# Performance work log

Hardware: AMD Instinct MI355X
Metric: run time of the kernel (lower is better)

The kernel has to match this reference:

```python
import jax, jax.numpy as jnp
import numpy as np

N = 50000
E = 800000
IN_C = 128
HID = 32
HEADS = 4
G = 512      # number of graphs in batch
OUT_C = 100
NEG_SLOPE = 0.2
EPS = 1e-16


def _gat_params(key, f_in, heads, c):
    k1, k2, k3, k4 = jax.random.split(key, 4)
    s = 1.0 / np.sqrt(f_in)
    return {
        'W': jax.random.uniform(k1, (heads * c, f_in), jnp.float32, -s, s),
        'att_src': jax.random.normal(k2, (heads, c), jnp.float32) * 0.1,
        'att_dst': jax.random.normal(k3, (heads, c), jnp.float32) * 0.1,
        'b': jnp.zeros((heads * c,), jnp.float32),
    }


def setup_inputs() -> dict:
    key = jax.random.key(0)
    ks = jax.random.split(key, 8)
    x = jax.random.normal(ks[0], (N, IN_C), jnp.float32)
    edge_index = jax.random.randint(ks[1], (2, E), 0, N, jnp.int64)
    batch = jnp.sort(jax.random.randint(ks[2], (N,), 0, G, jnp.int64))
    p1 = _gat_params(ks[3], IN_C, HEADS, HID)
    p2 = _gat_params(ks[4], HEADS * HID, HEADS, HID)
    p3 = _gat_params(ks[5], HEADS * HID, HEADS, HID)
    s = 1.0 / np.sqrt(HEADS * HID)
    fc_W = jax.random.uniform(ks[6], (OUT_C, HEADS * HID), jnp.float32, -s, s)
    fc_b = jnp.zeros((OUT_C,), jnp.float32)
    return {
        'x': x, 'edge_index': edge_index, 'batch': batch,
        'W1': p1['W'], 'as1': p1['att_src'], 'ad1': p1['att_dst'], 'b1': p1['b'],
        'W2': p2['W'], 'as2': p2['att_src'], 'ad2': p2['att_dst'], 'b2': p2['b'],
        'W3': p3['W'], 'as3': p3['att_src'], 'ad3': p3['att_dst'], 'b3': p3['b'],
        'fc_W': fc_W, 'fc_b': fc_b,
    }


def gat_conv(x, src, dst, W, att_src, att_dst, b):
    # x: [N, F_in] -> h: [N, H, C]
    h = (x @ W.T).reshape(N, HEADS, HID)
    a_src = jnp.einsum('nhc,hc->nh', h, att_src)   # [N, H]
    a_dst = jnp.einsum('nhc,hc->nh', h, att_dst)
    alpha = a_src[src] + a_dst[dst]                 # [E', H]
    alpha = jax.nn.leaky_relu(alpha, NEG_SLOPE)
    # segment softmax over incoming edges of each dst node
    m = jax.ops.segment_max(alpha, dst, num_segments=N)
    alpha = jnp.exp(alpha - m[dst])
    denom = jax.ops.segment_sum(alpha, dst, num_segments=N)
    alpha = alpha / (denom[dst] + EPS)
    msg = alpha[:, :, None] * h[src]                # [E', H, C]
    out = jax.ops.segment_sum(msg, dst, num_segments=N)
    return out.reshape(N, HEADS * HID) + b


def reference(x, edge_index, batch,
              W1, as1, ad1, b1, W2, as2, ad2, b2, W3, as3, ad3, b3,
              fc_W, fc_b):
    # add self loops (PyG GATConv default)
    loops = jnp.arange(N, dtype=edge_index.dtype)
    src = jnp.concatenate([edge_index[0], loops])
    dst = jnp.concatenate([edge_index[1], loops])
    h = jax.nn.elu(gat_conv(x, src, dst, W1, as1, ad1, b1))
    h = jax.nn.elu(gat_conv(h, src, dst, W2, as2, ad2, b2))
    h = jax.nn.elu(gat_conv(h, src, dst, W3, as3, ad3, b3))
    # global mean pool over graphs
    sums = jax.ops.segment_sum(h, batch, num_segments=G)        # [G, H*C]
    cnts = jax.ops.segment_sum(jnp.ones((N,), h.dtype), batch, num_segments=G)
    pooled = sums / jnp.maximum(cnts, 1.0)[:, None]
    # dropout p=0.5 is identity in eval mode
    return pooled @ fc_W.T + fc_b
```

## Files before the change

### kernel.cpp

```cpp
#include <hip/hip_runtime.h>
#include <math.h>

#define NN 50000
#define EE 800000
#define GG 512
#define OUTC 100
#define NEG 0.2f
#define STRIDE 64
#define NPART 8
#define PRNG (NN / NPART)
#define PCHUNK 4096

typedef __attribute__((ext_vector_type(8))) short bf16x8;
typedef __attribute__((ext_vector_type(8))) short s16x8;
typedef __attribute__((ext_vector_type(8))) unsigned short us8;
typedef __attribute__((ext_vector_type(4))) float f32x4;

__device__ inline ushort f2bf(float v) {
  unsigned u = __float_as_uint(v);
  unsigned r = (u + 0x7fff + ((u >> 16) & 1)) >> 16;
  return (ushort)r;
}

__global__ __launch_bounds__(256) void k_scatter(const int* __restrict__ ei,
    int* __restrict__ cursor, ushort* __restrict__ srcs) {
  int part = blockIdx.x & (NPART - 1);
  int chunk = blockIdx.x >> 3;
  int lo = part * PRNG, hi = lo + PRNG;
  int base = chunk * PCHUNK;
  for (int i = threadIdx.x; i < PCHUNK; i += 256) {
    int e = base + i;
    if (e >= EE) break;
    int d = ei[EE + e];
    if (d < lo || d >= hi) continue;
    int s = ei[e];
    int pos = atomicAdd(&cursor[d], 1);
    if (pos < STRIDE) srcs[(d << 6) + pos] = (ushort)s;
  }
}

__global__ __launch_bounds__(256) void k_prep(
    const float* __restrict__ W0, const float* __restrict__ W1, const float* __restrict__ W2,
    const float* __restrict__ as0, const float* __restrict__ as1, const float* __restrict__ as2,
    const float* __restrict__ ad0, const float* __restrict__ ad1, const float* __restrict__ ad2,
    ushort* __restrict__ hi, ushort* __restrict__ lo) {
  int layer = blockIdx.y;
  const float* W  = (layer == 0) ? W0 : (layer == 1) ? W1 : W2;
  const float* av = (layer == 0) ? as0 : (layer == 1) ? as1 : as2;
  const float* dv = (layer == 0) ? ad0 : (layer == 1) ? ad1 : ad2;
  ushort* hiL = hi + (size_t)layer * 144 * 128;
  ushort* loL = lo + (size_t)layer * 144 * 128;
  int idx = blockIdx.x * 256 + threadIdx.x;
  if (blockIdx.x < 64) {
    float v = W[idx];
    ushort hb = f2bf(v);
    float hf = __uint_as_float(((unsigned)hb) << 16);
    hiL[idx] = hb;
    loL[idx] = f2bf(v - hf);
  } else {
    int j2 = idx - 64 * 256;
    int j = j2 >> 7, k = j2 & 127;
    int head = j & 3;
    const float* vec = (j < 4) ? &av[head * 32] : &dv[head * 32];
    float dot = 0.f;
#pragma unroll
    for (int c = 0; c < 32; c++) dot += W[(head * 32 + c) * 128 + k] * vec[c];
    ushort hb = f2bf(dot);
    float hf = __uint_as_float(((unsigned)hb) << 16);
    hiL[(128 + j) * 128 + k] = hb;
    loL[(128 + j) * 128 + k] = f2bf(dot - hf);
    hiL[(136 + j) * 128 + k] = 0;
    loL[(136 + j) * 128 + k] = 0;
  }
}

__global__ __launch_bounds__(256) void k_gemm_mfma(const float* __restrict__ feat,
    const ushort* __restrict__ Whi, const ushort* __restrict__ Wlo,
    short* __restrict__ hq, float* __restrict__ scalef,
    float* __restrict__ asrcf, float* __restrict__ adstf) {
  __shared__ ushort Ahi[128 * 128];
  __shared__ ushort Alo[128 * 128];
  int n0 = blockIdx.x * 128;
  int t = threadIdx.x;
  {
    int row = t >> 1, half = t & 1;
    int n = n0 + row;
    int sw = row & 15;
    if (n < NN) {
      const float4* src = (const float4*)&feat[(size_t)n * 128 + half * 64];
#pragma unroll
      for (int i = 0; i < 8; i++) {
        float4 a = src[2 * i], b = src[2 * i + 1];
        float vv[8] = {a.x, a.y, a.z, a.w, b.x, b.y, b.z, b.w};
        us8 hh, ll;
#pragma unroll
        for (int j = 0; j < 8; j++) {
          ushort hb = f2bf(vv[j]);
          float hf = __uint_as_float(((unsigned)hb) << 16);
          hh[j] = hb;
          ll[j] = f2bf(vv[j] - hf);
        }
        int pc = (half * 8 + i) ^ sw;
        *(us8*)&Ahi[row * 128 + pc * 8] = hh;
        *(us8*)&Alo[row * 128 + pc * 8] = ll;
      }
    } else {
      us8 z = (us8)0;
#pragma unroll
      for (int i = 0; i < 8; i++) {
        int pc = (half * 8 + i) ^ sw;
        *(us8*)&Ahi[row * 128 + pc * 8] = z;
        *(us8*)&Alo[row * 128 + pc * 8] = z;
      }
    }
  }
  __syncthreads();

  int wave = t >> 6, lane = t & 63;
  int quad = lane >> 4, r16 = lane & 15;
  f32x4 acc[2][8];
#pragma unroll
  for (int mt = 0; mt < 2; mt++)
#pragma unroll
    for (int nt = 0; nt < 8; nt++) acc[mt][nt] = (f32x4)0.f;

  for (int ks = 0; ks < 4; ks++) {
    bf16x8 bh[8], bl[8];
#pragma unroll
    for (int nt = 0; nt < 8; nt++) {
      size_t wo = (size_t)(nt * 16 + r16) * 128 + ks * 32 + quad * 8;
      bh[nt] = *(const bf16x8*)&Whi[wo];
      bl[nt] = *(const bf16x8*)&Wlo[wo];
    }
#pragma unroll
    for (int mt = 0; mt < 2; mt++) {
      int row = wave * 32 + mt * 16 + r16;
      int pc = (ks * 4 + quad) ^ (row & 15);
      bf16x8 ah = *(const bf16x8*)&Ahi[row * 128 + pc * 8];
      bf16x8 al = *(const bf16x8*)&Alo[row * 128 + pc * 8];
#pragma unroll
      for (int nt = 0; nt < 8; nt++) {
        acc[mt][nt] = __builtin_amdgcn_mfma_f32_16x16x32_bf16(ah, bh[nt], acc[mt][nt], 0, 0, 0);
        acc[mt][nt] = __builtin_amdgcn_mfma_f32_16x16x32_bf16(al, bh[nt], acc[mt][nt], 0, 0, 0);
        acc[mt][nt] = __builtin_amdgcn_mfma_f32_16x16x32_bf16(ah, bl[nt], acc[mt][nt], 0, 0, 0);
      }
    }
  }

  f32x4 aug[2];
  aug[0] = (f32x4)0.f; aug[1] = (f32x4)0.f;
  for (int ks = 0; ks < 4; ks++) {
    size_t wo = (size_t)(128 + r16) * 128 + ks * 32 + quad * 8;
    bf16x8 bh = *(const bf16x8*)&Whi[wo];
    bf16x8 bl = *(const bf16x8*)&Wlo[wo];
#pragma unroll
    for (int mt = 0; mt < 2; mt++) {
      int row = wave * 32 + mt * 16 + r16;
      int pc = (ks * 4 + quad) ^ (row & 15);
      bf16x8 ah = *(const bf16x8*)&Ahi[row * 128 + pc * 8];
      bf16x8 al = *(const bf16x8*)&Alo[row * 128 + pc * 8];
      aug[mt] = __builtin_amdgcn_mfma_f32_16x16x32_bf16(ah, bh, aug[mt], 0, 0, 0);
      aug[mt] = __builtin_amdgcn_mfma_f32_16x16x32_bf16(al, bh, aug[mt], 0, 0, 0);
      aug[mt] = __builtin_amdgcn_mfma_f32_16x16x32_bf16(ah, bl, aug[mt], 0, 0, 0);
    }
  }

#pragma unroll
  for (int mt = 0; mt < 2; mt++) {
#pragma unroll
    for (int reg = 0; reg < 4; reg++) {
      float am = 0.f;
#pragma unroll
      for (int nt = 0; nt < 8; nt++) am = fmaxf(am, fabsf(acc[mt][nt][reg]));
#pragma unroll
      for (int off = 1; off < 16; off <<= 1) am = fmaxf(am, __shfl_xor(am, off));
      int node = n0 + wave * 32 + mt * 16 + quad * 4 + reg;
      if (node < NN) {
        float amc = fmaxf(am, 1e-20f);
        float rq = 32767.f / amc;
        if (r16 == 0) scalef[node] = amc * (1.f / 32767.f);
        if (r16 < 4) asrcf[node * 4 + r16] = aug[mt][reg];
        else if (r16 < 8) adstf[node * 4 + r16 - 4] = aug[mt][reg];
        short* dq = &hq[(size_t)node * 128 + r16];
#pragma unroll
        for (int nt = 0; nt < 8; nt++)
          dq[nt * 16] = (short)__float2int_rn(acc[mt][nt][reg] * rq);
      }
    }
  }
}

__global__ __launch_bounds__(256) void k_gather(const short* __restrict__ hq,
    const float* __restrict__ scalef,
    const float4* __restrict__ asrc, const float4* __restrict__ adst,
    const int* __restrict__ cursor, const ushort* __restrict__ srcs,
    const float* __restrict__ bias, float* __restrict__ outf) {
  __shared__ int s_src[4][4][16];
  __shared__ float s_w[4][4][72];
  __shared__ float s_e[4][4][72];

  int wave = threadIdx.x >> 6, lane = threadIdx.x & 63;
  int grp = lane >> 4;
  int gl = lane & 15;
  int node = blockIdx.x * 16 + wave * 4 + grp;

  int deg = 0, e0 = 0;
  float4 ad = make_float4(0.f, 0.f, 0.f, 0.f);
  if (node < NN) {
    deg = min(cursor[node], STRIDE);
    e0 = node << 6;
    ad = adst[node];
  }
  int c0 = gl << 3;
  int head = gl >> 2;

  float acc[8];
#pragma unroll
  for (int i = 0; i < 8; i++) acc[i] = 0.f;
  float wsum = 0.f;

  if (node < NN) {
    float4 a = asrc[node];
    float sc = scalef[node];
    float v, w0, w1, w2, w3;
    v = a.x + ad.x; v = v > 0.f ? v : NEG * v; w0 = expf(v);
    v = a.y + ad.y; v = v > 0.f ? v : NEG * v; w1 = expf(v);
    v = a.z + ad.z; v = v > 0.f ? v : NEG * v; w2 = expf(v);
    v = a.w + ad.w; v = v > 0.f ? v : NEG * v; w3 = expf(v);
    float wh = (head == 0) ? w0 : (head == 1) ? w1 : (head == 2) ? w2 : w3;
    wsum = wh;
    float ws = wh * sc;
    s16x8 qs = *(const s16x8*)&hq[(node << 7) + c0];
#pragma unroll
    for (int i = 0; i < 8; i++) acc[i] = ws * (float)qs[i];
  }

  int rounds = (deg + 15) >> 4;
  for (int r = 0; r < rounds; r++) {
    int base = r << 4;
    int j = base + gl;
    int sn = 0;
    float w0 = 0.f, w1 = 0.f, w2 = 0.f, w3 = 0.f, sc = 0.f;
    if (j < deg) {
      sn = srcs[e0 + j];
      float4 a = asrc[sn];
      sc = scalef[sn];
      float v;
      v = a.x + ad.x; v = v > 0.f ? v : NEG * v; w0 = expf(v);
      v = a.y + ad.y; v = v > 0.f ? v : NEG * v; w1 = expf(v);
      v = a.z + ad.z; v = v > 0.f ? v : NEG * v; w2 = expf(v);
      v = a.w + ad.w; v = v > 0.f ? v : NEG * v; w3 = expf(v);
    }
    s_src[wave][grp][gl] = sn << 7;
    float* wp = &s_w[wave][grp][gl << 2];
    wp[0] = w0 * sc; wp[1] = w1 * sc; wp[2] = w2 * sc; wp[3] = w3 * sc;
    float* ep = &s_e[wave][grp][gl << 2];
    ep[0] = w0; ep[1] = w1; ep[2] = w2; ep[3] = w3;
    __builtin_amdgcn_s_waitcnt(0);

    int cnt = min(16, deg - base);
    int cntp = (cnt + 3) & ~3;
    for (int k = 0; k < cntp; k += 4) {
      int ra = s_src[wave][grp][k + 0];
      int rb = s_src[wave][grp][k + 1];
      int rc = s_src[wave][grp][k + 2];
      int rd = s_src[wave][grp][k + 3];
      float wa = s_w[wave][grp][((k + 0) << 2) | head];
      float wb = s_w[wave][grp][((k + 1) << 2) | head];
      float wc = s_w[wave][grp][((k + 2) << 2) | head];
      float wd = s_w[wave][grp][((k + 3) << 2) | head];
      wsum += s_e[wave][grp][((k + 0) << 2) | head]
            + s_e[wave][grp][((k + 1) << 2) | head]
            + s_e[wave][grp][((k + 2) << 2) | head]
            + s_e[wave][grp][((k + 3) << 2) | head];
      s16x8 qa = *(const s16x8*)&hq[ra + c0];
      s16x8 qb = *(const s16x8*)&hq[rb + c0];
      s16x8 qc = *(const s16x8*)&hq[rc + c0];
      s16x8 qd = *(const s16x8*)&hq[rd + c0];
#pragma unroll
      for (int i = 0; i < 8; i++) acc[i] = fmaf(wa, (float)qa[i], acc[i]);
#pragma unroll
      for (int i = 0; i < 8; i++) acc[i] = fmaf(wb, (float)qb[i], acc[i]);
#pragma unroll
      for (int i = 0; i < 8; i++) acc[i] = fmaf(wc, (float)qc[i], acc[i]);
#pragma unroll
      for (int i = 0; i < 8; i++) acc[i] = fmaf(wd, (float)qd[i], acc[i]);
    }
  }

  if (node < NN) {
    float rcp = 1.f / (wsum + 1e-16f);
    float o[8];
#pragma unroll
    for (int i = 0; i < 8; i++) {
      float v = acc[i] * rcp + bias[c0 + i];
      o[i] = v > 0.f ? v : expm1f(v);
    }
    *(float4*)&outf[(size_t)node * 128 + c0] = make_float4(o[0], o[1], o[2], o[3]);
    *(float4*)&outf[(size_t)node * 128 + c0 + 4] = make_float4(o[4], o[5], o[6], o[7]);
  }
}

__global__ __launch_bounds__(128) void k_pool(const float* __restrict__ feat,
    const int* __restrict__ batch, float* __restrict__ pooled, float* __restrict__ cnt) {
  int n0 = blockIdx.x * 32;
  int c = threadIdx.x;
  float acc = 0.f; int curg = -1;
  for (int i = 0; i < 32; i++) {
    int n = n0 + i;
    if (n >= NN) break;
    int g = batch[n];
    if (g != curg) {
      if (curg >= 0) atomicAdd(&pooled[curg * 128 + c], acc);
      acc = 0.f; curg = g;
    }
    acc += feat[n * 128 + c];
  }
  if (curg >= 0) atomicAdd(&pooled[curg * 128 + c], acc);
  if (threadIdx.x == 0) {
    float cc = 0.f; int cg = -1;
    for (int i = 0; i < 32; i++) {
      int n = n0 + i;
      if (n >= NN) break;
      int g = batch[n];
      if (g != cg) { if (cg >= 0) atomicAdd(&cnt[cg], cc); cc = 0.f; cg = g; }
      cc += 1.f;
    }
    if (cg >= 0) atomicAdd(&cnt[cg], cc);
  }
}

__global__ __launch_bounds__(128) void k_fc(const float* __restrict__ pooled,
    const float* __restrict__ cnt, const float* __restrict__ fcW,
    const float* __restrict__ fcb, float* __restrict__ out) {
  int g = blockIdx.x;
  __shared__ float p[128];
  int t = threadIdx.x;
  float inv = 1.0f / fmaxf(cnt[g], 1.0f);
  p[t] = pooled[g * 128 + t] * inv;
  __syncthreads();
  if (t < OUTC) {
    float acc = fcb[t];
    const float4* wr = (const float4*)&fcW[t * 128];
    const float4* pp = (const float4*)p;
#pragma unroll
    for (int i = 0; i < 32; i++) {
      float4 w = wr[i], pv = pp[i];
      acc = fmaf(w.x, pv.x, fmaf(w.y, pv.y, fmaf(w.z, pv.z, fmaf(w.w, pv.w, acc))));
    }
    out[g * OUTC + t] = acc;
  }
}

extern "C" void kernel_launch(void* const* d_in, const int* in_sizes, int n_in,
                              void* d_out, int out_size, void* d_ws, size_t ws_size,
                              hipStream_t stream) {
  const float* x    = (const float*)d_in[0];
  const int*   ei   = (const int*)d_in[1];
  const int*   batch= (const int*)d_in[2];
  const float* W1   = (const float*)d_in[3];
  const float* as1  = (const float*)d_in[4];
  const float* ad1  = (const float*)d_in[5];
  const float* b1   = (const float*)d_in[6];
  const float* W2   = (const float*)d_in[7];
  const float* as2  = (const float*)d_in[8];
  const float* ad2  = (const float*)d_in[9];
  const float* b2   = (const float*)d_in[10];
  const float* W3   = (const float*)d_in[11];
  const float* as3  = (const float*)d_in[12];
  const float* ad3  = (const float*)d_in[13];
  const float* b3   = (const float*)d_in[14];
  const float* fcW  = (const float*)d_in[15];
  const float* fcb  = (const float*)d_in[16];
  float* out = (float*)d_out;

  char* p = (char*)d_ws;
  auto alloc = [&](size_t bytes) { char* r = p; p += (bytes + 255) & ~(size_t)255; return r; };
  short* hq     = (short*)alloc((size_t)NN * 128 * 2);
  float* scalef = (float*)alloc((size_t)NN * 4);
  float* buf0   = (float*)alloc((size_t)NN * 128 * 4);
  float* asrc   = (float*)alloc((size_t)NN * 4 * 4);
  float* adst   = (float*)alloc((size_t)NN * 4 * 4);
  char*  zbase  = p;
  int*   cursor = (int*)alloc((size_t)NN * 4);
  float* pooled = (float*)alloc((size_t)GG * 128 * 4);
  float* cnt    = (float*)alloc((size_t)GG * 4);
  size_t zlen   = (size_t)(p - zbase);
  ushort* srcs  = (ushort*)alloc((size_t)NN * STRIDE * 2);
  ushort* whi   = (ushort*)alloc((size_t)3 * 144 * 128 * 2);
  ushort* wlo   = (ushort*)alloc((size_t)3 * 144 * 128 * 2);

  hipMemsetAsync(zbase, 0, zlen, stream);

  int nchunks = (EE + PCHUNK - 1) / PCHUNK;
  k_scatter<<<NPART * nchunks, 256, 0, stream>>>(ei, cursor, srcs);
  k_prep<<<dim3(68, 3), 256, 0, stream>>>(W1, W2, W3, as1, as2, as3, ad1, ad2, ad3, whi, wlo);

  const float* bs[3] = {b1, b2, b3};
  const float* fin = x;
  for (int l = 0; l < 3; l++) {
    k_gemm_mfma<<<(NN + 127) / 128, 256, 0, stream>>>(fin,
        whi + (size_t)l * 144 * 128, wlo + (size_t)l * 144 * 128,
        hq, scalef, asrc, adst);
    k_gather<<<(NN + 15) / 16, 256, 0, stream>>>(hq, scalef,
        (const float4*)asrc, (const float4*)adst,
        cursor, srcs, bs[l], buf0);
    fin = buf0;
  }
  k_pool<<<(NN + 31) / 32, 128, 0, stream>>>(buf0, batch, pooled, cnt);
  k_fc<<<GG, 128, 0, stream>>>(pooled, cnt, fcW, fcb, out);
}
```

Measured before the change: 372.7 us.

## Load GEMM A fragments directly from global and widen gather unroll to 8

The projection GEMM drops the 64KB LDS staging of hi/lo bf16 A tiles. Each wave now loads its fragment straight from global and splits it in registers, and the attention-vector columns are folded into a ninth N-tile instead of running a separate loop. The low part is now truncated rather than rounded. The gather loop handles 8 neighbors per iteration instead of 4 to keep more random loads in flight. This should raise GEMM occupancy and remove an LDS round trip, at the cost of more VGPRs and more padded entries processed per gather chunk, which assumes the padding slots in shared memory hold zero weights.

```diff
diff --git a/kernel.cpp b/kernel.cpp
--- a/kernel.cpp
+++ b/kernel.cpp
@@ -78,90 +78,50 @@
     const ushort* __restrict__ Whi, const ushort* __restrict__ Wlo,
     short* __restrict__ hq, float* __restrict__ scalef,
     float* __restrict__ asrcf, float* __restrict__ adstf) {
-  __shared__ ushort Ahi[128 * 128];
-  __shared__ ushort Alo[128 * 128];
-  int n0 = blockIdx.x * 128;
   int t = threadIdx.x;
-  {
-    int row = t >> 1, half = t & 1;
-    int n = n0 + row;
-    int sw = row & 15;
-    if (n < NN) {
-      const float4* src = (const float4*)&feat[(size_t)n * 128 + half * 64];
-#pragma unroll
-      for (int i = 0; i < 8; i++) {
-        float4 a = src[2 * i], b = src[2 * i + 1];
-        float vv[8] = {a.x, a.y, a.z, a.w, b.x, b.y, b.z, b.w};
-        us8 hh, ll;
-#pragma unroll
-        for (int j = 0; j < 8; j++) {
-          ushort hb = f2bf(vv[j]);
-          float hf = __uint_as_float(((unsigned)hb) << 16);
-          hh[j] = hb;
-          ll[j] = f2bf(vv[j] - hf);
-        }
-        int pc = (half * 8 + i) ^ sw;
-        *(us8*)&Ahi[row * 128 + pc * 8] = hh;
-        *(us8*)&Alo[row * 128 + pc * 8] = ll;
-      }
-    } else {
-      us8 z = (us8)0;
-#pragma unroll
-      for (int i = 0; i < 8; i++) {
-        int pc = (half * 8 + i) ^ sw;
-        *(us8*)&Ahi[row * 128 + pc * 8] = z;
-        *(us8*)&Alo[row * 128 + pc * 8] = z;
-      }
-    }
-  }
-  __syncthreads();
-
   int wave = t >> 6, lane = t & 63;
   int quad = lane >> 4, r16 = lane & 15;
-  f32x4 acc[2][8];
+  int n0 = blockIdx.x * 128;
+
+  f32x4 acc[2][9];
 #pragma unroll
   for (int mt = 0; mt < 2; mt++)
 #pragma unroll
-    for (int nt = 0; nt < 8; nt++) acc[mt][nt] = (f32x4)0.f;
+    for (int nt = 0; nt < 9; nt++) acc[mt][nt] = (f32x4)0.f;
 
   for (int ks = 0; ks < 4; ks++) {
-    bf16x8 bh[8], bl[8];
-#pragma unroll
-    for (int nt = 0; nt < 8; nt++) {
-      size_t wo = (size_t)(nt * 16 + r16) * 128 + ks * 32 + quad * 8;
+    bf16x8 bh[9], bl[9];
+#pragma unroll
+    for (int nt = 0; nt < 9; nt++) {
+      int wrow = (nt < 8) ? (nt * 16 + r16) : (128 + r16);
+      size_t wo = (size_t)wrow * 128 + ks * 32 + quad * 8;
       bh[nt] = *(const bf16x8*)&Whi[wo];
       bl[nt] = *(const bf16x8*)&Wlo[wo];
     }
 #pragma unroll
     for (int mt = 0; mt < 2; mt++) {
-      int row = wave * 32 + mt * 16 + r16;
-      int pc = (ks * 4 + quad) ^ (row & 15);
-      bf16x8 ah = *(const bf16x8*)&Ahi[row * 128 + pc * 8];
-      bf16x8 al = *(const bf16x8*)&Alo[row * 128 + pc * 8];
-#pragma unroll
-      for (int nt = 0; nt < 8; nt++) {
+      int row = n0 + wave * 32 + mt * 16 + r16;
+      float4 va = make_float4(0.f, 0.f, 0.f, 0.f), vb = va;
+      if (row < NN) {
+        const float4* fp = (const float4*)&feat[(size_t)row * 128 + ks * 32 + quad * 8];
+        va = fp[0]; vb = fp[1];
+      }
+      float vv[8] = {va.x, va.y, va.z, va.w, vb.x, vb.y, vb.z, vb.w};
+      us8 hh, ll;
+#pragma unroll
+      for (int j = 0; j < 8; j++) {
+        ushort hb = f2bf(vv[j]);
+        float hf = __uint_as_float(((unsigned)hb) << 16);
+        hh[j] = hb;
+        ll[j] = (ushort)(__float_as_uint(vv[j] - hf) >> 16);
+      }
+      bf16x8 ah = (bf16x8)hh, al = (bf16x8)ll;
+#pragma unroll
+      for (int nt = 0; nt < 9; nt++) {
         acc[mt][nt] = __builtin_amdgcn_mfma_f32_16x16x32_bf16(ah, bh[nt], acc[mt][nt], 0, 0, 0);
         acc[mt][nt] = __builtin_amdgcn_mfma_f32_16x16x32_bf16(al, bh[nt], acc[mt][nt], 0, 0, 0);
         acc[mt][nt] = __builtin_amdgcn_mfma_f32_16x16x32_bf16(ah, bl[nt], acc[mt][nt], 0, 0, 0);
       }
-    }
-  }
-
-  f32x4 aug[2];
-  aug[0] = (f32x4)0.f; aug[1] = (f32x4)0.f;
-  for (int ks = 0; ks < 4; ks++) {
-    size_t wo = (size_t)(128 + r16) * 128 + ks * 32 + quad * 8;
-    bf16x8 bh = *(const bf16x8*)&Whi[wo];
-    bf16x8 bl = *(const bf16x8*)&Wlo[wo];
-#pragma unroll
-    for (int mt = 0; mt < 2; mt++) {
-      int row = wave * 32 + mt * 16 + r16;
-      int pc = (ks * 4 + quad) ^ (row & 15);
-      bf16x8 ah = *(const bf16x8*)&Ahi[row * 128 + pc * 8];
-      bf16x8 al = *(const bf16x8*)&Alo[row * 128 + pc * 8];
-      aug[mt] = __builtin_amdgcn_mfma_f32_16x16x32_bf16(ah, bh, aug[mt], 0, 0, 0);
-      aug[mt] = __builtin_amdgcn_mfma_f32_16x16x32_bf16(al, bh, aug[mt], 0, 0, 0);
-      aug[mt] = __builtin_amdgcn_mfma_f32_16x16x32_bf16(ah, bl, aug[mt], 0, 0, 0);
     }
   }
 
@@ -179,8 +139,8 @@
         float amc = fmaxf(am, 1e-20f);
         float rq = 32767.f / amc;
         if (r16 == 0) scalef[node] = amc * (1.f / 32767.f);
-        if (r16 < 4) asrcf[node * 4 + r16] = aug[mt][reg];
-        else if (r16 < 8) adstf[node * 4 + r16 - 4] = aug[mt][reg];
+        if (r16 < 4) asrcf[node * 4 + r16] = acc[mt][8][reg];
+        else if (r16 < 8) adstf[node * 4 + r16 - 4] = acc[mt][8][reg];
         short* dq = &hq[(size_t)node * 128 + r16];
 #pragma unroll
         for (int nt = 0; nt < 8; nt++)
@@ -259,32 +219,39 @@
     __builtin_amdgcn_s_waitcnt(0);
 
     int cnt = min(16, deg - base);
-    int cntp = (cnt + 3) & ~3;
-    for (int k = 0; k < cntp; k += 4) {
-      int ra = s_src[wave][grp][k + 0];
-      int rb = s_src[wave][grp][k + 1];
-      int rc = s_src[wave][grp][k + 2];
-      int rd = s_src[wave][grp][k + 3];
-      float wa = s_w[wave][grp][((k + 0) << 2) | head];
-      float wb = s_w[wave][grp][((k + 1) << 2) | head];
-      float wc = s_w[wave][grp][((k + 2) << 2) | head];
-      float wd = s_w[wave][grp][((k + 3) << 2) | head];
-      wsum += s_e[wave][grp][((k + 0) << 2) | head]
-            + s_e[wave][grp][((k + 1) << 2) | head]
-            + s_e[wave][grp][((k + 2) << 2) | head]
-            + s_e[wave][grp][((k + 3) << 2) | head];
-      s16x8 qa = *(const s16x8*)&hq[ra + c0];
-      s16x8 qb = *(const s16x8*)&hq[rb + c0];
-      s16x8 qc = *(const s16x8*)&hq[rc + c0];
-      s16x8 qd = *(const s16x8*)&hq[rd + c0];
-#pragma unroll
-      for (int i = 0; i < 8; i++) acc[i] = fmaf(wa, (float)qa[i], acc[i]);
-#pragma unroll
-      for (int i = 0; i < 8; i++) acc[i] = fmaf(wb, (float)qb[i], acc[i]);
-#pragma unroll
-      for (int i = 0; i < 8; i++) acc[i] = fmaf(wc, (float)qc[i], acc[i]);
-#pragma unroll
-      for (int i = 0; i < 8; i++) acc[i] = fmaf(wd, (float)qd[i], acc[i]);
+    int cntp = (cnt + 7) & ~7;
+    for (int k = 0; k < cntp; k += 8) {
+      int rr[8]; float ww[8];
+#pragma unroll
+      for (int u = 0; u < 8; u++) {
+        rr[u] = s_src[wave][grp][k + u];
+        ww[u] = s_w[wave][grp][((k + u) << 2) | head];
+        wsum += s_e[wave][grp][((k + u) << 2) | head];
+      }
+      s16x8 q0 = *(const s16x8*)&hq[rr[0] + c0];
+      s16x8 q1 = *(const s16x8*)&hq[rr[1] + c0];
+      s16x8 q2 = *(const s16x8*)&hq[rr[2] + c0];
+      s16x8 q3 = *(const s16x8*)&hq[rr[3] + c0];
+      s16x8 q4 = *(const s16x8*)&hq[rr[4] + c0];
+      s16x8 q5 = *(const s16x8*)&hq[rr[5] + c0];
+      s16x8 q6 = *(const s16x8*)&hq[rr[6] + c0];
+      s16x8 q7 = *(const s16x8*)&hq[rr[7] + c0];
+#pragma unroll
+      for (int i = 0; i < 8; i++) acc[i] = fmaf(ww[0], (float)q0[i], acc[i]);
+#pragma unroll
+      for (int i = 0; i < 8; i++) acc[i] = fmaf(ww[1], (float)q1[i], acc[i]);
+#pragma unroll
+      for (int i = 0; i < 8; i++) acc[i] = fmaf(ww[2], (float)q2[i], acc[i]);
+#pragma unroll
+      for (int i = 0; i < 8; i++) acc[i] = fmaf(ww[3], (float)q3[i], acc[i]);
+#pragma unroll
+      for (int i = 0; i < 8; i++) acc[i] = fmaf(ww[4], (float)q4[i], acc[i]);
+#pragma unroll
+      for (int i = 0; i < 8; i++) acc[i] = fmaf(ww[5], (float)q5[i], acc[i]);
+#pragma unroll
+      for (int i = 0; i < 8; i++) acc[i] = fmaf(ww[6], (float)q6[i], acc[i]);
+#pragma unroll
+      for (int i = 0; i < 8; i++) acc[i] = fmaf(ww[7], (float)q7[i], acc[i]);
     }
   }
 
```

Result: no change. 379.3 us (+1.8%).
